# Kernel tuning notes

Measured on AMD Instinct MI355X. Metric: run time of the kernel, lower is better.

## Reference

```python
import jax, jax.numpy as jnp
import numpy as np

DEPTH, DIM, HEADS, MLP, P, IMG, C = 6, 512, 8, 2048, 16, 224, 3
NPATCH = (IMG // P) ** 2  # 196
EPS = 1e-5


def setup_inputs() -> dict:
    key = jax.random.key(0)
    ks = jax.random.split(key, 16)
    s = 0.02
    return {
        "img": jax.random.normal(ks[0], (64, C, IMG, IMG), jnp.float32),
        "patch_w": jax.random.normal(ks[1], (DIM, C * P * P), jnp.float32) * s,
        "patch_b": jax.random.normal(ks[2], (DIM,), jnp.float32) * s,
        "cls_token": jax.random.normal(ks[3], (1, 1, DIM), jnp.float32),
        "pos_emb": jax.random.normal(ks[4], (1, NPATCH + 1, DIM), jnp.float32),
        "in_proj_w": jax.random.normal(ks[5], (DEPTH, 3 * DIM, DIM), jnp.float32) * s,
        "in_proj_b": jax.random.normal(ks[6], (DEPTH, 3 * DIM), jnp.float32) * s,
        "out_proj_w": jax.random.normal(ks[7], (DEPTH, DIM, DIM), jnp.float32) * s,
        "out_proj_b": jax.random.normal(ks[8], (DEPTH, DIM), jnp.float32) * s,
        "ln1_w": jnp.ones((DEPTH, DIM), jnp.float32),
        "ln1_b": jnp.zeros((DEPTH, DIM), jnp.float32),
        "fc1_w": jax.random.normal(ks[9], (DEPTH, MLP, DIM), jnp.float32) * s,
        "fc1_b": jax.random.normal(ks[10], (DEPTH, MLP), jnp.float32) * s,
        "fc2_w": jax.random.normal(ks[11], (DEPTH, DIM, MLP), jnp.float32) * s,
        "fc2_b": jax.random.normal(ks[12], (DEPTH, DIM), jnp.float32) * s,
        "ln2_w": jnp.ones((DEPTH, DIM), jnp.float32),
        "ln2_b": jnp.zeros((DEPTH, DIM), jnp.float32),
    }


def _ln(x, w, b):
    m = jnp.mean(x, -1, keepdims=True)
    v = jnp.mean(jnp.square(x - m), -1, keepdims=True)
    return (x - m) * jax.lax.rsqrt(v + EPS) * w + b


def _patchify(img):
    # b c (h p1) (w p2) -> b (h w) (p1 p2 c), lucidrains ViT ordering
    B = img.shape[0]
    g = IMG // P
    x = img.reshape(B, C, g, P, g, P)
    x = x.transpose(0, 2, 4, 3, 5, 1)  # B, h, w, p1, p2, c
    return x.reshape(B, g * g, P * P * C)


def _vit(img, patch_w, patch_b, cls_token, pos_emb, in_proj_w, in_proj_b,
         out_proj_w, out_proj_b, ln1_w, ln1_b, fc1_w, fc1_b, fc2_w, fc2_b,
         ln2_w, ln2_b):
    B = img.shape[0]
    hd = DIM // HEADS
    x = _patchify(img) @ patch_w.T + patch_b          # [B, 196, 512]
    cls = jnp.broadcast_to(cls_token, (B, 1, DIM))
    x = jnp.concatenate([cls, x], axis=1) + pos_emb   # [B, 197, 512]
    N = x.shape[1]
    for i in range(DEPTH):
        res = x
        qkv = x @ in_proj_w[i].T + in_proj_b[i]       # [B, N, 3*512]
        q, k, v = jnp.split(qkv, 3, axis=-1)
        q = q.reshape(B, N, HEADS, hd).transpose(0, 2, 1, 3)
        k = k.reshape(B, N, HEADS, hd).transpose(0, 2, 1, 3)
        v = v.reshape(B, N, HEADS, hd).transpose(0, 2, 1, 3)
        scores = jnp.einsum('bhnd,bhmd->bhnm', q, k) / jnp.sqrt(jnp.float32(hd))
        probs = jax.nn.softmax(scores, axis=-1)
        ctx = jnp.einsum('bhnm,bhmd->bhnd', probs, v)
        ctx = ctx.transpose(0, 2, 1, 3).reshape(B, N, DIM)
        x = ctx @ out_proj_w[i].T + out_proj_b[i] + res
        x = _ln(x, ln1_w[i], ln1_b[i])
        res = x
        h = jax.nn.gelu(x @ fc1_w[i].T + fc1_b[i], approximate=False)
        x = h @ fc2_w[i].T + fc2_b[i] + res
        x = _ln(x, ln2_w[i], ln2_b[i])
    return x[:, 0]  # ToCLS_Slice: forward returns CLS token [B, 512]


def reference(img, patch_w, patch_b, cls_token, pos_emb, in_proj_w, in_proj_b,
              out_proj_w, out_proj_b, ln1_w, ln1_b, fc1_w, fc1_b, fc2_w, fc2_b,
              ln2_w, ln2_b):
    return _vit(img, patch_w, patch_b, cls_token, pos_emb, in_proj_w, in_proj_b,
                out_proj_w, out_proj_b, ln1_w, ln1_b, fc1_w, fc1_b, fc2_w, fc2_b,
                ln2_w, ln2_b)
```

## Files before the change

### kernel.cpp

```cpp
#include <hip/hip_runtime.h>
#include <hip/hip_bf16.h>

typedef __hip_bfloat16 hb;
typedef __bf16 bf16x8 __attribute__((ext_vector_type(8)));
typedef float f32x4 __attribute__((ext_vector_type(4)));

#define N_DEPTH 6
#define N_DIM   512
#define N_HEADS 8
#define N_MLP   2048
#define N_TOK   197
#define N_PATCH 196
#define N_BATCH 64
#define ROWS    (N_BATCH * N_TOK)
#define ROWS_PAD 12672
#define PROWS   (N_BATCH * N_PATCH)

#define OFF_WPATCH 0u
#define OFF_WQKV   786432u
#define OFF_WOUT   10223616u
#define OFF_WFC1   13369344u
#define OFF_WFC2   25952256u
#define OFF_XBF    38535168u
#define OFF_CTX    51511296u
#define OFF_BIG    64487424u
#define OFF_XF     116391936u
#define OFF_H1     142344192u


__global__ void cvt_bf16_kernel(const float* __restrict__ in, hb* __restrict__ out, int n) {
    int t = blockIdx.x * 256 + threadIdx.x;
    if (t < n) out[t] = __float2bfloat16(in[t]);
}

__global__ void patchify_kernel(const float* __restrict__ img, hb* __restrict__ Xp) {
    int t = blockIdx.x * 256 + threadIdx.x;
    if (t >= PROWS * 768) return;
    int r = t / 768, j = t % 768;
    int b = r / 196, p = r % 196;
    int ph = p / 14, pw = p % 14;
    int p1 = j / 48, jr = j % 48;
    int p2 = jr / 3, c = jr % 3;
    float v = img[(((size_t)b * 3 + c) * 224 + ph * 16 + p1) * 224 + pw * 16 + p2];
    Xp[t] = __float2bfloat16(v);
}

__global__ void cls_init_kernel(const float* __restrict__ cls, const float* __restrict__ pos,
                                float* __restrict__ xf, hb* __restrict__ xb) {
    int t = blockIdx.x * 256 + threadIdx.x;
    int b = t >> 9, c = t & 511;
    float v = cls[c] + pos[c];
    size_t off = ((size_t)b * N_TOK) * N_DIM + c;
    xf[off] = v;
    xb[off] = __float2bfloat16(v);
}

__global__ void zero_pads_kernel(float* __restrict__ xf, hb* __restrict__ xb, hb* __restrict__ ctx) {
    int t = blockIdx.x * 256 + threadIdx.x;
    size_t off = (size_t)ROWS * N_DIM + t;
    xf[off] = 0.f;
    xb[off] = __float2bfloat16(0.f);
    ctx[off] = __float2bfloat16(0.f);
}

__global__ void extract_cls_kernel(const float* __restrict__ xf, float* __restrict__ out) {
    int t = blockIdx.x * 256 + threadIdx.x;
    int b = t >> 9, c = t & 511;
    out[t] = xf[((size_t)b * N_TOK) * N_DIM + c];
}


__global__ void __launch_bounds__(256) ln_kernel(const float* __restrict__ in,
                                                 const float* __restrict__ w, const float* __restrict__ b,
                                                 float* __restrict__ outf, hb* __restrict__ outb, int rows) {
    int row = blockIdx.x * 4 + (threadIdx.x >> 6);
    int lane = threadIdx.x & 63;
    if (row >= rows) return;
    const float* p = in + (size_t)row * N_DIM;
    float4 v0 = *(const float4*)(p + lane * 8);
    float4 v1 = *(const float4*)(p + lane * 8 + 4);
    float xs[8] = {v0.x, v0.y, v0.z, v0.w, v1.x, v1.y, v1.z, v1.w};
    float s = 0.f, q = 0.f;
#pragma unroll
    for (int j = 0; j < 8; ++j) { s += xs[j]; q += xs[j] * xs[j]; }
#pragma unroll
    for (int o = 32; o > 0; o >>= 1) { s += __shfl_xor(s, o); q += __shfl_xor(q, o); }
    float mean = s * (1.f / 512.f);
    float var = q * (1.f / 512.f) - mean * mean;
    float r = rsqrtf(var + 1e-5f);
    float4 w0 = *(const float4*)(w + lane * 8);
    float4 w1 = *(const float4*)(w + lane * 8 + 4);
    float4 b0 = *(const float4*)(b + lane * 8);
    float4 b1 = *(const float4*)(b + lane * 8 + 4);
    float ws8[8] = {w0.x, w0.y, w0.z, w0.w, w1.x, w1.y, w1.z, w1.w};
    float bs8[8] = {b0.x, b0.y, b0.z, b0.w, b1.x, b1.y, b1.z, b1.w};
    float of[8] __attribute__((aligned(16)));
    hb tb[8] __attribute__((aligned(16)));
#pragma unroll
    for (int j = 0; j < 8; ++j) {
        float y = (xs[j] - mean) * r * ws8[j] + bs8[j];
        of[j] = y;
        tb[j] = __float2bfloat16(y);
    }
    *(float4*)(outf + (size_t)row * N_DIM + lane * 8)     = *(const float4*)&of[0];
    *(float4*)(outf + (size_t)row * N_DIM + lane * 8 + 4) = *(const float4*)&of[4];
    *(float4*)(outb + (size_t)row * N_DIM + lane * 8)     = *(const float4*)&tb[0];
}


template <int MODE>
__global__ void __launch_bounds__(256) gemm_bt(const hb* __restrict__ A, const hb* __restrict__ B,
                                               const float* __restrict__ bias, int K, int N,
                                               hb* __restrict__ outb, float* __restrict__ outf,
                                               const float* __restrict__ res, const float* __restrict__ pos,
                                               hb* __restrict__ vtg) {
    __shared__ float4 As[512];
    __shared__ float4 Bs[512];
    const int tid = threadIdx.x;
    const int lane = tid & 63, wid = tid >> 6;
    const int wr = wid >> 1, wc = wid & 1;
    const int quad = lane >> 4, r16 = lane & 15;
    const int m0 = blockIdx.y * 128, n0 = blockIdx.x * 128;

    f32x4 acc[4][4] = {};

    for (int k0 = 0; k0 < K; k0 += 32) {
#pragma unroll
        for (int i = 0; i < 2; ++i) {
            int q = tid + (i << 8);
            int row = q >> 2, kc = q & 3;
            As[q] = *(const float4*)(A + (size_t)(m0 + row) * K + k0 + kc * 8);
            Bs[q] = *(const float4*)(B + (size_t)(n0 + row) * K + k0 + kc * 8);
        }
        __syncthreads();
        bf16x8 af[4], bfr[4];
#pragma unroll
        for (int t = 0; t < 4; ++t) {
            af[t]  = __builtin_bit_cast(bf16x8, As[(wr * 64 + t * 16 + r16) * 4 + quad]);
            bfr[t] = __builtin_bit_cast(bf16x8, Bs[(wc * 64 + t * 16 + r16) * 4 + quad]);
        }
#pragma unroll
        for (int mi = 0; mi < 4; ++mi)
#pragma unroll
            for (int nj = 0; nj < 4; ++nj)
                acc[mi][nj] = __builtin_amdgcn_mfma_f32_16x16x32_bf16(af[mi], bfr[nj], acc[mi][nj], 0, 0, 0);
        __syncthreads();
    }

    if constexpr (MODE == 0) {
        const bool isv = (n0 >= 1024);
#pragma unroll
        for (int mi = 0; mi < 4; ++mi) {
#pragma unroll
            for (int e = 0; e < 4; ++e) {
                int row = m0 + wr * 64 + mi * 16 + quad * 4 + e;
                int bb = row / 197;
                int mm = row - bb * 197;
#pragma unroll
                for (int nj = 0; nj < 4; ++nj) {
                    int col = n0 + wc * 64 + nj * 16 + r16;
                    float v = acc[mi][nj][e] + bias[col];
                    hb hv = __float2bfloat16(v);
                    outb[(size_t)row * N + col] = hv;
                    if (isv && bb < 64) {
                        int d = col - 1024;
                        vtg[((size_t)(bb * 8 + (d >> 6))) * (64 * 224) + (size_t)(d & 63) * 224 + mm] = hv;
                    }
                }
            }
        }
    } else {
#pragma unroll
        for (int nj = 0; nj < 4; ++nj) {
            int col = n0 + wc * 64 + nj * 16 + r16;
            float bv = bias[col];
#pragma unroll
            for (int mi = 0; mi < 4; ++mi) {
#pragma unroll
                for (int e = 0; e < 4; ++e) {
                    int row = m0 + wr * 64 + mi * 16 + quad * 4 + e;
                    float v = acc[mi][nj][e] + bv;
                    if constexpr (MODE == 1) {
                        v = 0.5f * v * (1.f + erff(v * 0.70710678118654752f));
                        outb[(size_t)row * N + col] = __float2bfloat16(v);
                    } else if constexpr (MODE == 2) {
                        v += res[(size_t)row * N + col];
                        outf[(size_t)row * N + col] = v;
                    } else {
                        int pidx = row % 196;
                        int row2 = row + row / 196 + 1;
                        v += pos[(size_t)(pidx + 1) * N_DIM + col];
                        outf[(size_t)row2 * N_DIM + col] = v;
                        outb[(size_t)row2 * N_DIM + col] = __float2bfloat16(v);
                    }
                }
            }
        }
    }
}


__global__ void __launch_bounds__(256, 2) attn_kernel(const hb* __restrict__ qkv,
                                                      const hb* __restrict__ vtg,
                                                      hb* __restrict__ ctx) {
    __shared__ hb Ks[224 * 64];
    __shared__ hb Vt[64 * 224];
    __shared__ hb Pb[4][16 * 40];
    const int bh = blockIdx.x;
    const int b = bh >> 3, h = bh & 7;
    const int tid = threadIdx.x, lane = tid & 63, wid = tid >> 6;
    const int quad = lane >> 4, r16 = lane & 15;
    const hb* base = qkv + (size_t)(b * N_TOK) * 1536 + h * 64;
    const hb* vbase = vtg + (size_t)bh * (64 * 224);

#pragma unroll
    for (int i = 0; i < 7; ++i) {
        int idx = tid + i * 256;
        int m = idx >> 3, c = idx & 7;
        bf16x8 val = {};
        if (m < 197) val = *(const bf16x8*)(base + (size_t)m * 1536 + 512 + c * 8);
        *(bf16x8*)&Ks[m * 64 + c * 8] = val;
    }
#pragma unroll
    for (int i = 0; i < 6; ++i) {
        int idx = tid + i * 256;
        int d = idx / 24, mc = idx % 24;
        *(bf16x8*)&Vt[d * 224 + mc * 8] = *(const bf16x8*)(vbase + d * 224 + mc * 8);
    }
    const hb hzero = __float2bfloat16(0.f);
#pragma unroll
    for (int i = 0; i < 8; ++i) {
        int idx = tid + i * 256;
        int d = idx >> 5, m = 192 + (idx & 31);
        Vt[d * 224 + m] = (m < 197) ? vbase[d * 224 + m] : hzero;
    }

    bf16x8 af[4][2];
#pragma unroll
    for (int mi = 0; mi < 4; ++mi) {
        int q = wid * 64 + mi * 16 + r16;
#pragma unroll
        for (int kc = 0; kc < 2; ++kc)
            af[mi][kc] = *(const bf16x8*)(base + (size_t)q * 1536 + kc * 32 + quad * 8);
    }

    f32x4 o[4][4] = {};
    float mst[4][4], lp[4][4];
#pragma unroll
    for (int mi = 0; mi < 4; ++mi)
#pragma unroll
        for (int e = 0; e < 4; ++e) { mst[mi][e] = -3.0e38f; lp[mi][e] = 0.f; }

    __syncthreads();

    for (int kt = 0; kt < 7; ++kt) {
        bf16x8 bk[2][2], bv[4];
#pragma unroll
        for (int nj = 0; nj < 2; ++nj)
#pragma unroll
            for (int kc = 0; kc < 2; ++kc)
                bk[nj][kc] = *(const bf16x8*)&Ks[(kt * 32 + nj * 16 + r16) * 64 + kc * 32 + quad * 8];
#pragma unroll
        for (int jd = 0; jd < 4; ++jd)
            bv[jd] = *(const bf16x8*)&Vt[(jd * 16 + r16) * 224 + kt * 32 + quad * 8];

        const bool v0 = (kt * 32 + r16) < N_TOK;
        const bool v1 = (kt * 32 + 16 + r16) < N_TOK;

#pragma unroll
        for (int mi = 0; mi < 4; ++mi) {
            f32x4 z = {};
            f32x4 s0v = __builtin_amdgcn_mfma_f32_16x16x32_bf16(af[mi][0], bk[0][0], z, 0, 0, 0);
            s0v = __builtin_amdgcn_mfma_f32_16x16x32_bf16(af[mi][1], bk[0][1], s0v, 0, 0, 0);
            f32x4 s1v = __builtin_amdgcn_mfma_f32_16x16x32_bf16(af[mi][0], bk[1][0], z, 0, 0, 0);
            s1v = __builtin_amdgcn_mfma_f32_16x16x32_bf16(af[mi][1], bk[1][1], s1v, 0, 0, 0);

            float al[4];
#pragma unroll
            for (int e = 0; e < 4; ++e) {
                float s0 = v0 ? s0v[e] * 0.125f : -1e30f;
                float s1 = v1 ? s1v[e] * 0.125f : -1e30f;
                float mx = fmaxf(s0, s1);
#pragma unroll
                for (int off = 1; off < 16; off <<= 1) mx = fmaxf(mx, __shfl_xor(mx, off));
                float mnew = fmaxf(mst[mi][e], mx);
                float alpha = __expf(mst[mi][e] - mnew);
                mst[mi][e] = mnew;
                float p0 = __expf(s0 - mnew);
                float p1 = __expf(s1 - mnew);
                lp[mi][e] = lp[mi][e] * alpha + p0 + p1;
                al[e] = alpha;
                int prow = (quad * 4 + e) * 40;
                Pb[wid][prow + r16]      = __float2bfloat16(p0);
                Pb[wid][prow + 16 + r16] = __float2bfloat16(p1);
            }
#pragma unroll
            for (int jd = 0; jd < 4; ++jd)
#pragma unroll
                for (int e = 0; e < 4; ++e) o[mi][jd][e] *= al[e];
            bf16x8 ap = *(const bf16x8*)&Pb[wid][r16 * 40 + quad * 8];
#pragma unroll
            for (int jd = 0; jd < 4; ++jd)
                o[mi][jd] = __builtin_amdgcn_mfma_f32_16x16x32_bf16(ap, bv[jd], o[mi][jd], 0, 0, 0);
        }
    }

#pragma unroll
    for (int mi = 0; mi < 4; ++mi) {
        float rl[4];
#pragma unroll
        for (int e = 0; e < 4; ++e) {
            float l = lp[mi][e];
#pragma unroll
            for (int off = 1; off < 16; off <<= 1) l += __shfl_xor(l, off);
            rl[e] = 1.f / l;
        }
        int qrow = wid * 64 + mi * 16 + quad * 4;
#pragma unroll
        for (int e = 0; e < 4; ++e) {
            int q = qrow + e;
            if (q < N_TOK) {
                hb* dst = ctx + ((size_t)(b * N_TOK + q)) * N_DIM + h * 64;
#pragma unroll
                for (int jd = 0; jd < 4; ++jd)
                    dst[jd * 16 + r16] = __float2bfloat16(o[mi][jd][e] * rl[e]);
            }
        }
    }
}


extern "C" void kernel_launch(void* const* d_in, const int* in_sizes, int n_in,
                              void* d_out, int out_size, void* d_ws, size_t ws_size,
                              hipStream_t stream) {
    (void)in_sizes; (void)n_in; (void)out_size; (void)ws_size;
    const float* img     = (const float*)d_in[0];
    const float* patch_w = (const float*)d_in[1];
    const float* patch_b = (const float*)d_in[2];
    const float* cls_t   = (const float*)d_in[3];
    const float* pos     = (const float*)d_in[4];
    const float* w_qkv   = (const float*)d_in[5];
    const float* b_qkv   = (const float*)d_in[6];
    const float* w_out   = (const float*)d_in[7];
    const float* b_out   = (const float*)d_in[8];
    const float* ln1w    = (const float*)d_in[9];
    const float* ln1b    = (const float*)d_in[10];
    const float* w_fc1   = (const float*)d_in[11];
    const float* b_fc1   = (const float*)d_in[12];
    const float* w_fc2   = (const float*)d_in[13];
    const float* b_fc2   = (const float*)d_in[14];
    const float* ln2w    = (const float*)d_in[15];
    const float* ln2b    = (const float*)d_in[16];

    char* ws = (char*)d_ws;
    hb* wPatch = (hb*)(ws + OFF_WPATCH);
    hb* wQKV   = (hb*)(ws + OFF_WQKV);
    hb* wOut   = (hb*)(ws + OFF_WOUT);
    hb* wFc1   = (hb*)(ws + OFF_WFC1);
    hb* wFc2   = (hb*)(ws + OFF_WFC2);
    hb* x_bf   = (hb*)(ws + OFF_XBF);
    hb* ctx    = (hb*)(ws + OFF_CTX);
    hb* Xp     = (hb*)(ws + OFF_BIG);
    hb* qkv    = (hb*)(ws + OFF_BIG);
    hb* hmid   = (hb*)(ws + OFF_BIG);
    float* x_f = (float*)(ws + OFF_XF);
    float* h1  = (float*)(ws + OFF_H1);
    hb* vtg    = (hb*)(ws + OFF_H1);

    auto cvt = [&](const float* src, hb* dst, int n) {
        cvt_bf16_kernel<<<dim3((n + 255) / 256), dim3(256), 0, stream>>>(src, dst, n);
    };
    cvt(patch_w, wPatch, 512 * 768);
    cvt(w_qkv, wQKV, N_DEPTH * 1536 * 512);
    cvt(w_out, wOut, N_DEPTH * 512 * 512);
    cvt(w_fc1, wFc1, N_DEPTH * 2048 * 512);
    cvt(w_fc2, wFc2, N_DEPTH * 512 * 2048);

    patchify_kernel<<<dim3((PROWS * 768 + 255) / 256), dim3(256), 0, stream>>>(img, Xp);
    gemm_bt<3><<<dim3(4, 98), dim3(256), 0, stream>>>(Xp, wPatch, patch_b, 768, 512, x_bf, x_f, nullptr, pos, nullptr);
    cls_init_kernel<<<dim3(128), dim3(256), 0, stream>>>(cls_t, pos, x_f, x_bf);
    zero_pads_kernel<<<dim3(128), dim3(256), 0, stream>>>(x_f, x_bf, ctx);

    for (int i = 0; i < N_DEPTH; ++i) {
        gemm_bt<0><<<dim3(12, 99), dim3(256), 0, stream>>>(x_bf, wQKV + (size_t)i * 1536 * 512,
                                                           b_qkv + i * 1536, 512, 1536, qkv, nullptr, nullptr, nullptr, vtg);
        attn_kernel<<<dim3(512), dim3(256), 0, stream>>>(qkv, vtg, ctx);
        gemm_bt<2><<<dim3(4, 99), dim3(256), 0, stream>>>(ctx, wOut + (size_t)i * 512 * 512,
                                                          b_out + i * 512, 512, 512, nullptr, h1, x_f, nullptr, nullptr);
        ln_kernel<<<dim3(3152), dim3(256), 0, stream>>>(h1, ln1w + i * 512, ln1b + i * 512, x_f, x_bf, ROWS);
        gemm_bt<1><<<dim3(16, 99), dim3(256), 0, stream>>>(x_bf, wFc1 + (size_t)i * 2048 * 512,
                                                           b_fc1 + i * 2048, 512, 2048, hmid, nullptr, nullptr, nullptr, nullptr);
        gemm_bt<2><<<dim3(4, 99), dim3(256), 0, stream>>>(hmid, wFc2 + (size_t)i * 512 * 2048,
                                                          b_fc2 + i * 512, 2048, 512, nullptr, h1, x_f, nullptr, nullptr);
        ln_kernel<<<dim3(3152), dim3(256), 0, stream>>>(h1, ln2w + i * 512, ln2b + i * 512, x_f, x_bf, ROWS);
    }

    extract_cls_kernel<<<dim3(128), dim3(256), 0, stream>>>(x_f, (float*)d_out);
}
```

Baseline: 1.782 ms.

## Load GEMM tiles via global_load_lds and stage bf16 epilogue through LDS

Replaces the register-staged global-to-LDS tile copy in the bf16 GEMM with direct global_load_lds DMA, so tile data no longer passes through VGPRs. For the QKV (non-V columns) and GELU modes, the epilogue now writes results into LDS per warp and emits coalesced 16-byte row stores instead of scattered 2-byte stores. The LDS layout changes to a row-major 32-wide bf16 tile, which may add LDS bank conflicts on the fragment reads. There is still no double buffering, so the loads are not overlapped with the MFMA work.

```diff
diff --git a/kernel.cpp b/kernel.cpp
--- a/kernel.cpp
+++ b/kernel.cpp
@@ -26,6 +26,11 @@
 #define OFF_BIG    64487424u
 #define OFF_XF     116391936u
 #define OFF_H1     142344192u
+
+__device__ __forceinline__ void gl2lds(const hb* g, hb* l) {
+    __builtin_amdgcn_global_load_lds((const __attribute__((address_space(1))) unsigned int*)g,
+                                     (__attribute__((address_space(3))) unsigned int*)l, 16, 0, 0);
+}
 
 
 __global__ void cvt_bf16_kernel(const float* __restrict__ in, hb* __restrict__ out, int n) {
@@ -114,30 +119,39 @@
                                                hb* __restrict__ outb, float* __restrict__ outf,
                                                const float* __restrict__ res, const float* __restrict__ pos,
                                                hb* __restrict__ vtg) {
-    __shared__ float4 As[512];
-    __shared__ float4 Bs[512];
+    __shared__ hb Sm[8192];
+    hb* As = Sm;
+    hb* Bs = Sm + 4096;
     const int tid = threadIdx.x;
     const int lane = tid & 63, wid = tid >> 6;
     const int wr = wid >> 1, wc = wid & 1;
     const int quad = lane >> 4, r16 = lane & 15;
     const int m0 = blockIdx.y * 128, n0 = blockIdx.x * 128;
 
+    const int r0 = lane >> 2, c0 = lane & 3;
+    const hb* ga0 = A + (size_t)(m0 + wid * 32 + r0) * K + c0 * 8;
+    const hb* ga1 = ga0 + (size_t)16 * K;
+    const hb* gb0 = B + (size_t)(n0 + wid * 32 + r0) * K + c0 * 8;
+    const hb* gb1 = gb0 + (size_t)16 * K;
+    hb* la0 = As + (wid * 32) * 32;
+    hb* la1 = As + (wid * 32 + 16) * 32;
+    hb* lb0 = Bs + (wid * 32) * 32;
+    hb* lb1 = Bs + (wid * 32 + 16) * 32;
+
     f32x4 acc[4][4] = {};
 
     for (int k0 = 0; k0 < K; k0 += 32) {
-#pragma unroll
-        for (int i = 0; i < 2; ++i) {
-            int q = tid + (i << 8);
-            int row = q >> 2, kc = q & 3;
-            As[q] = *(const float4*)(A + (size_t)(m0 + row) * K + k0 + kc * 8);
-            Bs[q] = *(const float4*)(B + (size_t)(n0 + row) * K + k0 + kc * 8);
-        }
+        gl2lds(ga0, la0);
+        gl2lds(ga1, la1);
+        gl2lds(gb0, lb0);
+        gl2lds(gb1, lb1);
+        ga0 += 32; ga1 += 32; gb0 += 32; gb1 += 32;
         __syncthreads();
         bf16x8 af[4], bfr[4];
 #pragma unroll
         for (int t = 0; t < 4; ++t) {
-            af[t]  = __builtin_bit_cast(bf16x8, As[(wr * 64 + t * 16 + r16) * 4 + quad]);
-            bfr[t] = __builtin_bit_cast(bf16x8, Bs[(wc * 64 + t * 16 + r16) * 4 + quad]);
+            af[t]  = *(const bf16x8*)&As[(wr * 64 + t * 16 + r16) * 32 + quad * 8];
+            bfr[t] = *(const bf16x8*)&Bs[(wc * 64 + t * 16 + r16) * 32 + quad * 8];
         }
 #pragma unroll
         for (int mi = 0; mi < 4; ++mi)
@@ -147,24 +161,52 @@
         __syncthreads();
     }
 
-    if constexpr (MODE == 0) {
-        const bool isv = (n0 >= 1024);
-#pragma unroll
-        for (int mi = 0; mi < 4; ++mi) {
-#pragma unroll
-            for (int e = 0; e < 4; ++e) {
-                int row = m0 + wr * 64 + mi * 16 + quad * 4 + e;
-                int bb = row / 197;
-                int mm = row - bb * 197;
-#pragma unroll
-                for (int nj = 0; nj < 4; ++nj) {
-                    int col = n0 + wc * 64 + nj * 16 + r16;
-                    float v = acc[mi][nj][e] + bias[col];
-                    hb hv = __float2bfloat16(v);
-                    outb[(size_t)row * N + col] = hv;
-                    if (isv && bb < 64) {
-                        int d = col - 1024;
-                        vtg[((size_t)(bb * 8 + (d >> 6))) * (64 * 224) + (size_t)(d & 63) * 224 + mm] = hv;
+    if constexpr (MODE == 0 || MODE == 1) {
+        const bool isv = (MODE == 0) && (n0 >= 1024);
+        if (!isv) {
+            hb* Cb = Sm + wid * 2048;
+#pragma unroll
+            for (int p = 0; p < 2; ++p) {
+#pragma unroll
+                for (int nj2 = 0; nj2 < 2; ++nj2) {
+                    int nj = p * 2 + nj2;
+                    float bv = bias[n0 + wc * 64 + nj * 16 + r16];
+#pragma unroll
+                    for (int mi = 0; mi < 4; ++mi)
+#pragma unroll
+                        for (int e = 0; e < 4; ++e) {
+                            float v = acc[mi][nj][e] + bv;
+                            if constexpr (MODE == 1)
+                                v = 0.5f * v * (1.f + erff(v * 0.70710678118654752f));
+                            Cb[(mi * 16 + quad * 4 + e) * 32 + nj2 * 16 + r16] = __float2bfloat16(v);
+                        }
+                }
+#pragma unroll
+                for (int it = 0; it < 4; ++it) {
+                    int idx = it * 64 + lane;
+                    int row = idx >> 2, ch = idx & 3;
+                    bf16x8 val = *(const bf16x8*)&Cb[row * 32 + ch * 8];
+                    *(bf16x8*)(outb + (size_t)(m0 + wr * 64 + row) * N + n0 + wc * 64 + p * 32 + ch * 8) = val;
+                }
+            }
+        } else {
+#pragma unroll
+            for (int mi = 0; mi < 4; ++mi) {
+#pragma unroll
+                for (int e = 0; e < 4; ++e) {
+                    int row = m0 + wr * 64 + mi * 16 + quad * 4 + e;
+                    int bb = row / 197;
+                    int mm = row - bb * 197;
+#pragma unroll
+                    for (int nj = 0; nj < 4; ++nj) {
+                        int col = n0 + wc * 64 + nj * 16 + r16;
+                        float v = acc[mi][nj][e] + bias[col];
+                        hb hv = __float2bfloat16(v);
+                        outb[(size_t)row * N + col] = hv;
+                        if (bb < 64) {
+                            int d = col - 1024;
+                            vtg[((size_t)(bb * 8 + (d >> 6))) * (64 * 224) + (size_t)(d & 63) * 224 + mm] = hv;
+                        }
                     }
                 }
             }
@@ -180,10 +222,7 @@
                 for (int e = 0; e < 4; ++e) {
                     int row = m0 + wr * 64 + mi * 16 + quad * 4 + e;
                     float v = acc[mi][nj][e] + bv;
-                    if constexpr (MODE == 1) {
-                        v = 0.5f * v * (1.f + erff(v * 0.70710678118654752f));
-                        outb[(size_t)row * N + col] = __float2bfloat16(v);
-                    } else if constexpr (MODE == 2) {
+                    if constexpr (MODE == 2) {
                         v += res[(size_t)row * N + col];
                         outf[(size_t)row * N + col] = v;
                     } else {
```

Result: faster. 1.746 ms (-2.0%).
